# Kernel tuning notes

Measured on AMD Instinct MI355X. Metric: run time of the kernel, lower is better.

Reference implementation:

```python
import math
import jax, jax.numpy as jnp
import numpy as np

V, D, A, H, FF, L, MD = 500, 512, 512, 8, 2048, 6, 512
HD = A // H
B, S, T = 32, 512, 128


def setup_inputs() -> dict:
    key = jax.random.key(0)
    ks = jax.random.split(key, 40)
    init = lambda k, shape: (jax.random.normal(k, shape, jnp.float32) * 0.02)
    inp = {
        'memory': jax.random.normal(ks[0], (B, S, MD), jnp.float32),
        'memory_lens': jax.random.randint(ks[1], (B,), S // 2, S + 1),
        'ys_in_pad': jax.random.randint(ks[2], (B, T), 0, V),
        'ys_in_lens': jax.random.randint(ks[3], (B,), T // 2, T + 1),
        'emb': init(ks[4], (V, D)),
        'w_out': init(ks[5], (D, V)),
        'b_out': jnp.zeros((V,), jnp.float32),
        # per-layer params stacked on leading L axis (consumed by lax.scan)
        'ln_sa_g': jnp.ones((L, D), jnp.float32), 'ln_sa_b': jnp.zeros((L, D), jnp.float32),
        'sa_wq': init(ks[6], (L, D, A)), 'sa_bq': init(ks[7], (L, A)),
        'sa_wk': init(ks[8], (L, D, A)), 'sa_bk': init(ks[9], (L, A)),
        'sa_wv': init(ks[10], (L, D, A)), 'sa_bv': init(ks[11], (L, A)),
        'sa_wo': init(ks[12], (L, A, D)), 'sa_bo': init(ks[13], (L, D)),
        'ln_ca_g': jnp.ones((L, D), jnp.float32), 'ln_ca_b': jnp.zeros((L, D), jnp.float32),
        'ca_wq': init(ks[14], (L, D, A)), 'ca_bq': init(ks[15], (L, A)),
        'ca_wk': init(ks[16], (L, MD, A)), 'ca_bk': init(ks[17], (L, A)),
        'ca_wv': init(ks[18], (L, MD, A)), 'ca_bv': init(ks[19], (L, A)),
        'ca_wo': init(ks[20], (L, A, D)), 'ca_bo': init(ks[21], (L, D)),
        'ln_ff_g': jnp.ones((L, D), jnp.float32), 'ln_ff_b': jnp.zeros((L, D), jnp.float32),
        'ff_w1': init(ks[22], (L, D, FF)), 'ff_b1': init(ks[23], (L, FF)),
        'ff_w2': init(ks[24], (L, FF, D)), 'ff_b2': init(ks[25], (L, D)),
    }
    return inp


def _layernorm(x, g, b, eps=1e-5):
    m = jnp.mean(x, axis=-1, keepdims=True)
    v = jnp.mean(jnp.square(x - m), axis=-1, keepdims=True)
    return (x - m) * jax.lax.rsqrt(v + eps) * g + b


def _mha(q_in, k_in, v_in, mask, wq, bq, wk, bk, wv, bv, wo, bo):
    # mask: True = disallowed. (B, T, S) for self-attn, (B, 1, S) for cross-attn.
    b_, tq, _ = q_in.shape
    ts = k_in.shape[1]
    q = (q_in @ wq + bq).reshape(b_, tq, H, HD).transpose(0, 2, 1, 3)
    k = (k_in @ wk + bk).reshape(b_, ts, H, HD).transpose(0, 2, 1, 3)
    v = (v_in @ wv + bv).reshape(b_, ts, H, HD).transpose(0, 2, 1, 3)
    s = jnp.einsum('bhtd,bhsd->bhts', q, k) / math.sqrt(HD)
    # penalize_abs_values_gt(limit=50, penalty=1e-4) is identity in the forward
    # pass (it only injects an auxiliary gradient during training).
    s = jnp.where(mask[:, None, :, :], -jnp.inf, s)
    a = jax.nn.softmax(s, axis=-1)  # dropout p=0.0 in this config
    o = jnp.einsum('bhts,bhsd->bhtd', a, v).transpose(0, 2, 1, 3).reshape(b_, tq, A)
    return o @ wo + bo


def _forward(memory, memory_lens, ys_in_pad, ys_in_lens, emb, w_out, b_out, layer_params):
    t = ys_in_pad.shape[1]
    # make_pad_mask | ~subsequent_mask  -> (B, T, T), True = masked
    pad = jnp.arange(t)[None, :] >= ys_in_lens[:, None]            # (B, T)
    causal = ~jnp.tril(jnp.ones((t, t), bool))                     # (T, T)
    tgt_mask = pad[:, None, :] | causal[None]                      # (B, T, T)
    mem_mask = (jnp.arange(memory.shape[1])[None, :] >= memory_lens[:, None])[:, None, :]

    # embedding + sinusoidal positional encoding (dropout in eval = identity)
    pos = jnp.arange(t, dtype=jnp.float32)[:, None]
    div = jnp.exp(jnp.arange(0, D, 2, dtype=jnp.float32) * (-math.log(10000.0) / D))
    pe = jnp.zeros((t, D), jnp.float32)
    pe = pe.at[:, 0::2].set(jnp.sin(pos * div)).at[:, 1::2].set(jnp.cos(pos * div))
    x = emb[ys_in_pad] * math.sqrt(D) + pe[None]

    def step(tgt, p):
        tn = _layernorm(tgt, p['ln_sa_g'], p['ln_sa_b'])
        tgt = tgt + _mha(tn, tn, tn, tgt_mask,
                         p['sa_wq'], p['sa_bq'], p['sa_wk'], p['sa_bk'],
                         p['sa_wv'], p['sa_bv'], p['sa_wo'], p['sa_bo'])
        tn = _layernorm(tgt, p['ln_ca_g'], p['ln_ca_b'])
        tgt = tgt + _mha(tn, memory, memory, mem_mask,
                         p['ca_wq'], p['ca_bq'], p['ca_wk'], p['ca_bk'],
                         p['ca_wv'], p['ca_bv'], p['ca_wo'], p['ca_bo'])
        tn = _layernorm(tgt, p['ln_ff_g'], p['ln_ff_b'])
        h = tn @ p['ff_w1'] + p['ff_b1']
        h = h * jax.nn.sigmoid(h)  # Swish
        tgt = tgt + h @ p['ff_w2'] + p['ff_b2']
        return tgt, None

    x, _ = jax.lax.scan(step, x, layer_params)
    return x @ w_out + b_out  # (B, T, V) logits


_LAYER_KEYS = ['ln_sa_g', 'ln_sa_b', 'sa_wq', 'sa_bq', 'sa_wk', 'sa_bk', 'sa_wv', 'sa_bv',
               'sa_wo', 'sa_bo', 'ln_ca_g', 'ln_ca_b', 'ca_wq', 'ca_bq', 'ca_wk', 'ca_bk',
               'ca_wv', 'ca_bv', 'ca_wo', 'ca_bo', 'ln_ff_g', 'ln_ff_b',
               'ff_w1', 'ff_b1', 'ff_w2', 'ff_b2']


def reference(memory, memory_lens, ys_in_pad, ys_in_lens, emb, w_out, b_out,
              ln_sa_g, ln_sa_b, sa_wq, sa_bq, sa_wk, sa_bk, sa_wv, sa_bv, sa_wo, sa_bo,
              ln_ca_g, ln_ca_b, ca_wq, ca_bq, ca_wk, ca_bk, ca_wv, ca_bv, ca_wo, ca_bo,
              ln_ff_g, ln_ff_b, ff_w1, ff_b1, ff_w2, ff_b2):
    loc = locals()
    layer_params = {k: loc[k] for k in _LAYER_KEYS}
    return _forward(memory, memory_lens, ys_in_pad, ys_in_lens, emb, w_out, b_out, layer_params)
```

## Files before the change

kernel.cpp:

```cpp
#include <hip/hip_runtime.h>
#include <hip/hip_bf16.h>
#include <hip/hip_fp16.h>

constexpr int Bc = 32, Sc = 512, Tc = 128, Dc = 512, Ac = 512, Hc = 8;
constexpr int HDc = 64, FFc = 2048, Lc = 6, Vc = 500;
constexpr int NTOK = Bc * Tc;
constexpr int NMEM = Bc * Sc;

typedef unsigned short u16;
typedef __attribute__((ext_vector_type(8))) short short8;
typedef __attribute__((ext_vector_type(4))) float f32x4;

__device__ __forceinline__ u16 bfc(float x) {
  __hip_bfloat16 h = __float2bfloat16(x);
  return *reinterpret_cast<u16*>(&h);
}

__device__ __forceinline__ void gload16(const void* g, void* l) {
  __builtin_amdgcn_global_load_lds(
      (const __attribute__((address_space(1))) unsigned int*)g,
      (__attribute__((address_space(3))) unsigned int*)l, 16, 0, 0);
}

template <int N>
__device__ __forceinline__ void waitv() {
  if constexpr (N == 8)      asm volatile("s_waitcnt vmcnt(8)" ::: "memory");
  else if constexpr (N == 6) asm volatile("s_waitcnt vmcnt(6)" ::: "memory");
  else if constexpr (N == 4) asm volatile("s_waitcnt vmcnt(4)" ::: "memory");
  else if constexpr (N == 3) asm volatile("s_waitcnt vmcnt(3)" ::: "memory");
  else                       asm volatile("s_waitcnt vmcnt(0)" ::: "memory");
  __builtin_amdgcn_sched_barrier(0);
}
__device__ __forceinline__ void barrier_fenced() {
  __builtin_amdgcn_s_barrier();
  __builtin_amdgcn_sched_barrier(0);
}
__device__ __forceinline__ void lgk0_barrier() {
  asm volatile("s_waitcnt lgkmcnt(0)" ::: "memory");
  __builtin_amdgcn_sched_barrier(0);
  __builtin_amdgcn_s_barrier();
  __builtin_amdgcn_sched_barrier(0);
}

__device__ __forceinline__ float wave_sum(float v) {
#pragma unroll
  for (int o = 32; o > 0; o >>= 1) v += __shfl_down(v, o);
  return v;
}
__device__ __forceinline__ float wave_max(float v) {
#pragma unroll
  for (int o = 32; o > 0; o >>= 1) v = fmaxf(v, __shfl_down(v, o));
  return v;
}

__global__ __launch_bounds__(256) void embed_pe_k(const int* __restrict__ ys,
                                                  const float* __restrict__ emb,
                                                  float* __restrict__ x) {
  int tok = blockIdx.x;
  int t = tok & (Tc - 1);
  int id = ys[tok];
  int j = threadIdx.x;
  int d0 = 2 * j;
  const float cdiv = -9.210340371976184f / (float)Dc;
  float div = expf((float)d0 * cdiv);
  float ang = (float)t * div;
  float pe0 = sinf(ang), pe1 = cosf(ang);
  const float sc = 22.627416997969522f;
  long base = (long)tok * Dc + d0;
  long ebase = (long)id * Dc + d0;
  x[base]     = emb[ebase]     * sc + pe0;
  x[base + 1] = emb[ebase + 1] * sc + pe1;
}

__global__ __launch_bounds__(256) void layernorm_k(const float* __restrict__ x,
                                                   const float* __restrict__ g,
                                                   const float* __restrict__ bta,
                                                   u16* __restrict__ out) {
  int row = blockIdx.x;
  int tid = threadIdx.x;
  const float* xr = x + (long)row * Dc;
  float2 xv = *(const float2*)(xr + tid * 2);
  float s  = xv.x + xv.y;
  float s2 = xv.x * xv.x + xv.y * xv.y;
  __shared__ float red[4], red2[4];
#pragma unroll
  for (int o = 32; o > 0; o >>= 1) {
    s  += __shfl_down(s, o);
    s2 += __shfl_down(s2, o);
  }
  if ((tid & 63) == 0) { red[tid >> 6] = s; red2[tid >> 6] = s2; }
  __syncthreads();
  float mean = (red[0] + red[1] + red[2] + red[3]) * (1.0f / Dc);
  float ms   = (red2[0] + red2[1] + red2[2] + red2[3]) * (1.0f / Dc);
  float var  = ms - mean * mean;
  float rstd = rsqrtf(var + 1e-5f);
  float dx0 = xv.x - mean, dx1 = xv.y - mean;
  ushort2 o;
  o.x = bfc(dx0 * rstd * g[2 * tid] + bta[2 * tid]);
  o.y = bfc(dx1 * rstd * g[2 * tid + 1] + bta[2 * tid + 1]);
  *(ushort2*)(out + (long)row * Dc + tid * 2) = o;
}

__global__ __launch_bounds__(256) void wtrans_k(const float* __restrict__ src,
                                                u16* __restrict__ dst,
                                                int K, int N, long srcStride, long dstStride) {
  int z = blockIdx.z;
  src += z * srcStride;
  dst += z * dstStride;
  __shared__ float t[32][33];
  int n0 = blockIdx.x * 32, k0 = blockIdx.y * 32;
  int tx = threadIdx.x & 31, ty = threadIdx.x >> 5;
#pragma unroll
  for (int i = 0; i < 4; i++) {
    int n = n0 + tx;
    t[ty + 8 * i][tx] = (n < N) ? src[(long)(k0 + ty + 8 * i) * N + n] : 0.0f;
  }
  __syncthreads();
#pragma unroll
  for (int i = 0; i < 4; i++) {
    dst[(long)(n0 + ty + 8 * i) * K + k0 + tx] = bfc(t[tx][ty + 8 * i]);
  }
}

struct PtrPack8 { const float* p[8]; };
__global__ __launch_bounds__(256) void wtrans8_k(PtrPack8 P, u16* __restrict__ Wt,
                                                 long PLW) {
  int z = blockIdx.z;
  int widx = z / 6, l = z - widx * 6;
  const float* src = P.p[widx] + (long)l * 262144;
  u16* dst = Wt + (long)widx * 262144 + (long)l * PLW;
  __shared__ float t[32][33];
  int n0 = blockIdx.x * 32, k0 = blockIdx.y * 32;
  int tx = threadIdx.x & 31, ty = threadIdx.x >> 5;
#pragma unroll
  for (int i = 0; i < 4; i++)
    t[ty + 8 * i][tx] = src[(long)(k0 + ty + 8 * i) * 512 + n0 + tx];
  __syncthreads();
#pragma unroll
  for (int i = 0; i < 4; i++)
    dst[(long)(n0 + ty + 8 * i) * 512 + k0 + tx] = bfc(t[tx][ty + 8 * i]);
}

__global__ __launch_bounds__(256) void f2b_k(const float* __restrict__ in,
                                             u16* __restrict__ out, long n) {
  long i = ((long)blockIdx.x * 256 + threadIdx.x) * 4;
  if (i >= n) return;
  float4 v = *(const float4*)(in + i);
  ushort4 o;
  o.x = bfc(v.x); o.y = bfc(v.y); o.z = bfc(v.z); o.w = bfc(v.w);
  *(ushort4*)(out + i) = o;
}

template <int BMW, int OMODE, bool BIAS, bool RES, bool SWISH, bool NCH, bool MLEN>
__global__ __launch_bounds__(256) void mgemm_k(
    const u16* __restrict__ A, const u16* __restrict__ Bt,
    const float* __restrict__ bias0, const float* __restrict__ bias1,
    const float* __restrict__ bias2,
    void* __restrict__ Cv, const float* __restrict__ R, const int* __restrict__ mlens,
    int N, int K, int lda, int ldb, int ldc, int nbi,
    long batAo, long batAi, long batBo, long batBi, long batCo, long batCi) {
  constexpr int BM = BMW * 32;
  constexpr int LPS = (BM == 128 ? 2 : 1) + 2;

  int gx = gridDim.x, gy = gridDim.y;
  int nwg = gx * gy * gridDim.z;
  int orig = blockIdx.x + gx * (blockIdx.y + gy * blockIdx.z);
  int q = nwg >> 3, r = nwg & 7, xcd = orig & 7, off = orig >> 3;
  int wgid = (xcd < r ? xcd * (q + 1) : r * (q + 1) + (xcd - r) * q) + off;
  int bxi = wgid % gx; int tmp = wgid / gx;
  int byi = tmp % gy;  int bzi = tmp / gy;

  int z = bzi;
  int bo = z / nbi, bi = z - bo * nbi;
  int m0 = byi * BM, n0 = bxi * 128;

  if constexpr (MLEN) {
    if ((m0 & 511) >= mlens[m0 >> 9]) return;
  }

  const u16* Ab = A + bo * batAo + bi * batAi;
  const u16* Bb = Bt + bo * batBo + bi * batBi;
  long coff = bo * batCo + bi * batCi;
  const float* bias = nullptr;
  if constexpr (BIAS) bias = (bi == 0) ? bias0 : ((bi == 1) ? bias1 : bias2);

  __shared__ __align__(16) u16 As[3][BM * 32];
  __shared__ __align__(16) u16 Bs[3][128 * 32];

  int tid = threadIdx.x;
  int lane = tid & 63, wid = tid >> 6;
  int wm = wid >> 1, wn = wid & 1;
  int fr = lane & 15, grp = lane >> 4;

  f32x4 acc[BMW][4];
#pragma unroll
  for (int i = 0; i < BMW; i++)
#pragma unroll
    for (int j = 0; j < 4; j++) acc[i][j] = (f32x4){0.f, 0.f, 0.f, 0.f};

  const u16* ga = Ab + (long)(m0 + (tid >> 2)) * lda + ((tid & 3) << 3);
  const u16* gb = Bb + (long)(n0 + (tid >> 2)) * ldb + ((tid & 3) << 3);

  auto STAGE = [&](int buf, int kt) {
    u16* lA = &As[buf][tid * 8];
    u16* lB = &Bs[buf][tid * 8];
    gload16(ga + kt, lA);
    if constexpr (BM == 128) gload16(ga + kt + (long)64 * lda, lA + 2048);
    gload16(gb + kt, lB);
    gload16(gb + kt + (long)64 * ldb, lB + 2048);
  };

  auto COMPUTE = [&](int buf) {
    short8 av[BMW], bv[4];
#pragma unroll
    for (int i = 0; i < BMW; i++)
      av[i] = *(const short8*)&As[buf][(wm * BMW * 16 + i * 16 + fr) * 32 + grp * 8];
#pragma unroll
    for (int j = 0; j < 4; j++)
      bv[j] = *(const short8*)&Bs[buf][(wn * 64 + j * 16 + fr) * 32 + grp * 8];
#pragma unroll
    for (int i = 0; i < BMW; i++)
#pragma unroll
      for (int j = 0; j < 4; j++)
        acc[i][j] = __builtin_amdgcn_mfma_f32_16x16x32_bf16(av[i], bv[j], acc[i][j], 0, 0, 0);
  };

  int NT = K >> 5;
  STAGE(0, 0);
  STAGE(1, 32);
  int cbuf = 0, sbuf = 2, kt = 64;
  for (int t = 0; t < NT - 2; ++t) {
    STAGE(sbuf, kt); kt += 32;
    waitv<2 * LPS>();
    barrier_fenced();
    COMPUTE(cbuf);
    lgk0_barrier();
    sbuf = cbuf; cbuf = (cbuf == 2) ? 0 : cbuf + 1;
  }
  waitv<LPS>();  barrier_fenced(); COMPUTE(cbuf); lgk0_barrier();
  cbuf = (cbuf == 2) ? 0 : cbuf + 1;
  waitv<0>();    barrier_fenced(); COMPUTE(cbuf);

  int rbase = m0 + wm * BMW * 16 + grp * 4;
  int cbase = n0 + wn * 64 + fr;
#pragma unroll
  for (int i = 0; i < BMW; i++) {
#pragma unroll
    for (int j = 0; j < 4; j++) {
      int col = cbase + j * 16;
      if (NCH && col >= N) continue;
      float bb = 0.0f;
      if constexpr (BIAS) bb = bias[col];
#pragma unroll
      for (int r2 = 0; r2 < 4; r2++) {
        int row = rbase + i * 16 + r2;
        float v = acc[i][j][r2] + bb;
        long idx = coff + (long)row * ldc + col;
        if constexpr (RES) v += R[idx];
        if constexpr (SWISH) v = v / (1.0f + expf(-v));
        if constexpr (OMODE == 0) ((u16*)Cv)[idx] = bfc(v);
        else ((float*)Cv)[idx] = v;
      }
    }
  }
}

template <int SKV, int KVBLK, bool CAUSAL, int IQ>
__global__ __launch_bounds__(256) void fattn_k(
    const u16* __restrict__ Q, const u16* __restrict__ Kg, const u16* __restrict__ Vg,
    u16* __restrict__ O, const int* __restrict__ lens) {
  constexpr int NJ  = KVBLK / 16;
  constexpr int NKV = KVBLK / 32;
  constexpr int NT  = SKV / KVBLK;
  constexpr int KST = 72;
  constexpr int VST = KVBLK + 8;
  constexpr int WR  = 16 * IQ;
  constexpr int WGR = 64 * IQ;
  constexpr int CH  = KVBLK / 32;

  __shared__ __align__(16) u16 Ks[KVBLK * KST];
  __shared__ __align__(16) u16 Vs[64 * VST];
  __shared__ __align__(16) u16 Ps[WGR * VST];

  int bh = blockIdx.x; int b = bh >> 3, h = bh & 7;
  int row00 = blockIdx.y * WGR;
  int tid = threadIdx.x, lane = tid & 63, wid = tid >> 6;
  int fr = lane & 15, grp = lane >> 4;
  int len = lens[b];
  int row0w = row00 + wid * WR;

  short8 qa[IQ][2];
  {
    const u16* qp = Q + ((long)b * Tc + row0w + fr) * 512 + h * 64 + grp * 8;
#pragma unroll
    for (int i = 0; i < IQ; i++)
#pragma unroll
      for (int k2 = 0; k2 < 2; k2++)
        qa[i][k2] = *(const short8*)(qp + (long)i * 16 * 512 + k2 * 32);
  }

  float m_run[IQ][4], l_run[IQ][4];
  f32x4 acc_o[IQ][4];
#pragma unroll
  for (int i = 0; i < IQ; i++)
#pragma unroll
    for (int r = 0; r < 4; r++) { m_run[i][r] = -1e30f; l_run[i][r] = 0.0f; }
#pragma unroll
  for (int i = 0; i < IQ; i++)
#pragma unroll
    for (int j = 0; j < 4; j++) acc_o[i][j] = (f32x4){0.f, 0.f, 0.f, 0.f};

  const u16* Kbase = Kg + ((long)b * SKV) * 512 + h * 64;
  const u16* Vbase = Vg + ((long)b * SKV) * 512 + h * 64;

  int NTeff = NT;
  if constexpr (CAUSAL) NTeff = (row00 + WGR - 1) / KVBLK + 1;
  int lenT = (len + KVBLK - 1) / KVBLK;
  if (lenT < NTeff) NTeff = lenT;

  short8 kreg[CH], vreg[CH];
#pragma unroll
  for (int c = 0; c < CH; c++) {
    int idx = tid + 256 * c; int kv = idx >> 3, s = idx & 7;
    kreg[c] = *(const short8*)(Kbase + (long)kv * 512 + s * 8);
    vreg[c] = *(const short8*)(Vbase + (long)kv * 512 + s * 8);
  }

  for (int t = 0; t < NTeff; t++) {
    int kv0 = t * KVBLK;
    __syncthreads();
#pragma unroll
    for (int c = 0; c < CH; c++) {
      int idx = tid + 256 * c; int kv = idx >> 3, s = idx & 7;
      *(short8*)&Ks[kv * KST + s * 8] = kreg[c];
#pragma unroll
      for (int j = 0; j < 8; j++)
        Vs[(s * 8 + j) * VST + kv] = (u16)vreg[c][j];
    }
    __syncthreads();
    if (t + 1 < NTeff) {
      int kvn = kv0 + KVBLK;
#pragma unroll
      for (int c = 0; c < CH; c++) {
        int idx = tid + 256 * c; int kv = idx >> 3, s = idx & 7;
        kreg[c] = *(const short8*)(Kbase + (long)(kvn + kv) * 512 + s * 8);
        vreg[c] = *(const short8*)(Vbase + (long)(kvn + kv) * 512 + s * 8);
      }
    }

    int jmax = NJ;
    if constexpr (CAUSAL) {
      jmax = (row0w + WR - 1 - kv0) / 16 + 1;
      if (jmax > NJ) jmax = NJ;
    }

    f32x4 accs[IQ][NJ];
    __builtin_amdgcn_s_setprio(1);
#pragma unroll
    for (int j = 0; j < NJ; j++) {
      if (CAUSAL && j >= jmax) continue;
      short8 bv0 = *(const short8*)&Ks[(j * 16 + fr) * KST + grp * 8];
      short8 bv1 = *(const short8*)&Ks[(j * 16 + fr) * KST + 32 + grp * 8];
#pragma unroll
      for (int i = 0; i < IQ; i++) {
        f32x4 a = __builtin_amdgcn_mfma_f32_16x16x32_bf16(qa[i][0], bv0, (f32x4){0.f,0.f,0.f,0.f}, 0, 0, 0);
        accs[i][j] = __builtin_amdgcn_mfma_f32_16x16x32_bf16(qa[i][1], bv1, a, 0, 0, 0);
      }
    }
    __builtin_amdgcn_s_setprio(0);

    float alpha[IQ][4];
#pragma unroll
    for (int i = 0; i < IQ; i++) {
#pragma unroll
      for (int r = 0; r < 4; r++) {
        int qrow = row0w + i * 16 + grp * 4 + r;
        float vmax = -1e30f;
#pragma unroll
        for (int j = 0; j < NJ; j++) {
          if (CAUSAL && j >= jmax) continue;
          int kvb = kv0 + j * 16 + fr;
          float s = accs[i][j][r] * 0.125f;
          bool msk = (kvb >= len) || (CAUSAL && kvb > qrow);
          s = msk ? -1e30f : s;
          accs[i][j][r] = s;
          vmax = fmaxf(vmax, s);
        }
        vmax = fmaxf(vmax, __shfl_xor(vmax, 1));
        vmax = fmaxf(vmax, __shfl_xor(vmax, 2));
        vmax = fmaxf(vmax, __shfl_xor(vmax, 4));
        vmax = fmaxf(vmax, __shfl_xor(vmax, 8));
        float mn = fmaxf(m_run[i][r], vmax);
        float al = __expf(m_run[i][r] - mn);
        m_run[i][r] = mn;
        alpha[i][r] = al;
        float rs = 0.0f;
#pragma unroll
        for (int j = 0; j < NJ; j++) {
          if (CAUSAL && j >= jmax) continue;
          float p = __expf(accs[i][j][r] - mn);
          accs[i][j][r] = p;
          rs += p;
        }
        rs += __shfl_xor(rs, 1);
        rs += __shfl_xor(rs, 2);
        rs += __shfl_xor(rs, 4);
        rs += __shfl_xor(rs, 8);
        l_run[i][r] = l_run[i][r] * al + rs;
      }
    }

#pragma unroll
    for (int i = 0; i < IQ; i++)
#pragma unroll
      for (int j = 0; j < NJ; j++) {
        if (CAUSAL && j >= jmax) continue;
#pragma unroll
        for (int r = 0; r < 4; r++) {
          int prow = wid * WR + i * 16 + grp * 4 + r;
          Ps[prow * VST + j * 16 + fr] = bfc(accs[i][j][r]);
        }
      }

#pragma unroll
    for (int i = 0; i < IQ; i++)
#pragma unroll
      for (int jd = 0; jd < 4; jd++)
#pragma unroll
        for (int r = 0; r < 4; r++)
          acc_o[i][jd][r] *= alpha[i][r];

    int kvmax = NKV;
    if constexpr (CAUSAL) {
      kvmax = (row0w + WR - 1 - kv0) / 32 + 1;
      if (kvmax > NKV) kvmax = NKV;
    }
    __builtin_amdgcn_s_setprio(1);
#pragma unroll
    for (int kk = 0; kk < NKV; kk++) {
      if (CAUSAL && kk >= kvmax) continue;
      short8 pa[IQ];
#pragma unroll
      for (int i = 0; i < IQ; i++)
        pa[i] = *(const short8*)&Ps[(wid * WR + i * 16 + fr) * VST + kk * 32 + grp * 8];
#pragma unroll
      for (int jd = 0; jd < 4; jd++) {
        short8 vb = *(const short8*)&Vs[(jd * 16 + fr) * VST + kk * 32 + grp * 8];
#pragma unroll
        for (int i = 0; i < IQ; i++)
          acc_o[i][jd] = __builtin_amdgcn_mfma_f32_16x16x32_bf16(pa[i], vb, acc_o[i][jd], 0, 0, 0);
      }
    }
    __builtin_amdgcn_s_setprio(0);
  }

#pragma unroll
  for (int i = 0; i < IQ; i++) {
#pragma unroll
    for (int r = 0; r < 4; r++) {
      float inv = 1.0f / l_run[i][r];
      long tok = (long)b * Tc + row0w + i * 16 + grp * 4 + r;
#pragma unroll
      for (int jd = 0; jd < 4; jd++)
        O[tok * 512 + h * 64 + jd * 16 + fr] = bfc(acc_o[i][jd][r] * inv);
    }
  }
}

extern "C" void kernel_launch(void* const* d_in, const int* in_sizes, int n_in,
                              void* d_out, int out_size, void* d_ws, size_t ws_size,
                              hipStream_t stream) {
  const float* memory   = (const float*)d_in[0];
  const int*   mem_lens = (const int*)d_in[1];
  const int*   ys       = (const int*)d_in[2];
  const int*   ys_lens  = (const int*)d_in[3];
  const float* emb      = (const float*)d_in[4];
  const float* w_out    = (const float*)d_in[5];
  const float* b_out    = (const float*)d_in[6];
  const float* pp[26];
  for (int i = 0; i < 26; i++) pp[i] = (const float*)d_in[7 + i];

  constexpr long PLW = 4194304;
  constexpr long OFF_SAQ = 0, OFF_SAK = 262144, OFF_SAV = 524288, OFF_SAO = 786432,
                 OFF_CAQ = 1048576, OFF_CAK = 1310720, OFF_CAV = 1572864,
                 OFF_CAO = 1835008, OFF_FF1 = 2097152, OFF_FF2 = 3145728,
                 OFF_WOUT = 6 * PLW;
  u16*   Wt   = (u16*)d_ws;
  float* X    = (float*)(Wt + 25427968);
  u16*   TO   = (u16*)(X + 2097152);
  u16*   QKV  = TO + 2097152;
  u16*   memb = QKV + 3 * 2097152;
  u16*   Kb   = memb + 8388608;
  u16*   SCR  = Kb + 8388608;
  float* OUT  = (float*)d_out;

  PtrPack8 P8;
  P8.p[0] = pp[2];  P8.p[1] = pp[4];  P8.p[2] = pp[6];  P8.p[3] = pp[8];
  P8.p[4] = pp[12]; P8.p[5] = pp[14]; P8.p[6] = pp[16]; P8.p[7] = pp[18];
  wtrans8_k<<<dim3(16, 16, 48), 256, 0, stream>>>(P8, Wt, PLW);
  wtrans_k<<<dim3(64, 16, Lc), 256, 0, stream>>>(pp[22], Wt + OFF_FF1, 512, 2048, 1048576, PLW);
  wtrans_k<<<dim3(16, 64, Lc), 256, 0, stream>>>(pp[24], Wt + OFF_FF2, 2048, 512, 1048576, PLW);
  wtrans_k<<<dim3(16, 16, 1), 256, 0, stream>>>(w_out, Wt + OFF_WOUT, 512, 500, 0, 0);

  f2b_k<<<(NMEM * Dc / 4 + 255) / 256, 256, 0, stream>>>(memory, memb, (long)NMEM * Dc);
  embed_pe_k<<<NTOK, 256, 0, stream>>>(ys, emb, X);

  for (int l = 0; l < Lc; l++) {
    const u16* WtL = Wt + (long)l * PLW;

    layernorm_k<<<NTOK, 256, 0, stream>>>(X, pp[0] + (long)l * Dc, pp[1] + (long)l * Dc, TO);
    mgemm_k<4, 0, true, false, false, false, false><<<dim3(4, 32, 3), 256, 0, stream>>>(
        TO, WtL + OFF_SAQ, pp[3] + (long)l * Ac, pp[5] + (long)l * Ac, pp[7] + (long)l * Ac,
        QKV, nullptr, nullptr, 512, 512, 512, 512, 512, 3, 0, 0, 0, 262144, 0, 2097152);
    fattn_k<128, 128, true, 2><<<dim3(256, 1), 256, 0, stream>>>(
        QKV, QKV + 2097152, QKV + 2 * 2097152, TO, ys_lens);
    mgemm_k<2, 1, true, true, false, false, false><<<dim3(4, 64, 1), 256, 0, stream>>>(
        TO, WtL + OFF_SAO, pp[9] + (long)l * Dc, nullptr, nullptr, X, X, nullptr,
        512, 512, 512, 512, 512, 1, 0, 0, 0, 0, 0, 0);

    layernorm_k<<<NTOK, 256, 0, stream>>>(X, pp[10] + (long)l * Dc, pp[11] + (long)l * Dc, TO);
    mgemm_k<2, 0, true, false, false, false, false><<<dim3(4, 64, 1), 256, 0, stream>>>(
        TO, WtL + OFF_CAQ, pp[13] + (long)l * Ac, nullptr, nullptr, QKV, nullptr, nullptr,
        512, 512, 512, 512, 512, 1, 0, 0, 0, 0, 0, 0);
    mgemm_k<4, 0, true, false, false, false, true><<<dim3(4, 128, 2), 256, 0, stream>>>(
        memb, WtL + OFF_CAK, pp[15] + (long)l * Ac, pp[17] + (long)l * Ac, nullptr,
        Kb, nullptr, mem_lens, 512, 512, 512, 512, 512, 2, 0, 0, 0, 262144, 0, 8388608);
    fattn_k<512, 128, false, 1><<<dim3(256, 2), 256, 0, stream>>>(
        QKV, Kb, SCR, TO, mem_lens);
    mgemm_k<2, 1, true, true, false, false, false><<<dim3(4, 64, 1), 256, 0, stream>>>(
        TO, WtL + OFF_CAO, pp[19] + (long)l * Dc, nullptr, nullptr, X, X, nullptr,
        512, 512, 512, 512, 512, 1, 0, 0, 0, 0, 0, 0);

    layernorm_k<<<NTOK, 256, 0, stream>>>(X, pp[20] + (long)l * Dc, pp[21] + (long)l * Dc, TO);
    mgemm_k<4, 0, true, false, true, false, false><<<dim3(16, 32, 1), 256, 0, stream>>>(
        TO, WtL + OFF_FF1, pp[23] + (long)l * FFc, nullptr, nullptr, SCR, nullptr, nullptr,
        2048, 512, 512, 512, 2048, 1, 0, 0, 0, 0, 0, 0);
    mgemm_k<2, 1, true, true, false, false, false><<<dim3(4, 64, 1), 256, 0, stream>>>(
        SCR, WtL + OFF_FF2, pp[25] + (long)l * Dc, nullptr, nullptr, X, X, nullptr,
        512, 2048, 2048, 2048, 512, 1, 0, 0, 0, 0, 0, 0);
  }

  f2b_k<<<(NTOK * Dc / 4 + 255) / 256, 256, 0, stream>>>(X, TO, (long)NTOK * Dc);
  mgemm_k<2, 1, true, false, false, true, false><<<dim3(4, 64, 1), 256, 0, stream>>>(
      TO, Wt + OFF_WOUT, b_out, nullptr, nullptr, OUT, nullptr, nullptr,
      500, 512, 512, 512, 500, 1, 0, 0, 0, 0, 0, 0);
}
```

Baseline: 1.185 ms.

## Deepen GEMM pipeline to 4 stages, merge cross-attn Q/KV GEMMs, split causal attention

The GEMM kernel moves from triple to quadruple LDS buffering, keeping three tiles in flight to hide more global-load latency. The cross-attention Q projection and the memory K/V projections are merged into one launch with a MERGE mode that selects input and output per z-slice. Causal self-attention now runs with one query tile per wave over a two-dimensional grid, zeroing masked P columns so the PV loop stays aligned. In exchange, LDS use grows, which may lower occupancy, and the merged launch contains idle blocks for Q rows beyond 4096.

```diff
diff --git a/kernel.cpp b/kernel.cpp
--- a/kernel.cpp
+++ b/kernel.cpp
@@ -24,7 +24,9 @@
 
 template <int N>
 __device__ __forceinline__ void waitv() {
-  if constexpr (N == 8)      asm volatile("s_waitcnt vmcnt(8)" ::: "memory");
+  if constexpr (N == 12)     asm volatile("s_waitcnt vmcnt(12)" ::: "memory");
+  else if constexpr (N == 9) asm volatile("s_waitcnt vmcnt(9)" ::: "memory");
+  else if constexpr (N == 8) asm volatile("s_waitcnt vmcnt(8)" ::: "memory");
   else if constexpr (N == 6) asm volatile("s_waitcnt vmcnt(6)" ::: "memory");
   else if constexpr (N == 4) asm volatile("s_waitcnt vmcnt(4)" ::: "memory");
   else if constexpr (N == 3) asm volatile("s_waitcnt vmcnt(3)" ::: "memory");
@@ -45,11 +47,6 @@
 __device__ __forceinline__ float wave_sum(float v) {
 #pragma unroll
   for (int o = 32; o > 0; o >>= 1) v += __shfl_down(v, o);
-  return v;
-}
-__device__ __forceinline__ float wave_max(float v) {
-#pragma unroll
-  for (int o = 32; o > 0; o >>= 1) v = fmaxf(v, __shfl_down(v, o));
   return v;
 }
 
@@ -151,12 +148,13 @@
   *(ushort4*)(out + i) = o;
 }
 
-template <int BMW, int OMODE, bool BIAS, bool RES, bool SWISH, bool NCH, bool MLEN>
+template <int BMW, int OMODE, bool BIAS, bool RES, bool SWISH, bool NCH, bool MLEN, bool MERGE>
 __global__ __launch_bounds__(256) void mgemm_k(
     const u16* __restrict__ A, const u16* __restrict__ Bt,
     const float* __restrict__ bias0, const float* __restrict__ bias1,
     const float* __restrict__ bias2,
     void* __restrict__ Cv, const float* __restrict__ R, const int* __restrict__ mlens,
+    const u16* __restrict__ A2, void* __restrict__ Cv2, int Mq,
     int N, int K, int lda, int ldb, int ldc, int nbi,
     long batAo, long batAi, long batBo, long batBi, long batCo, long batCi) {
   constexpr int BM = BMW * 32;
@@ -174,18 +172,33 @@
   int bo = z / nbi, bi = z - bo * nbi;
   int m0 = byi * BM, n0 = bxi * 128;
 
-  if constexpr (MLEN) {
-    if ((m0 & 511) >= mlens[m0 >> 9]) return;
-  }
-
-  const u16* Ab = A + bo * batAo + bi * batAi;
+  const u16* Ab;
+  long coff;
+  void* Cbase;
+  if constexpr (MERGE) {
+    if (bi == 0) {
+      if (m0 >= Mq) return;
+      Ab = A + (long)0;
+      coff = 0; Cbase = Cv;
+    } else {
+      if (MLEN && (m0 & 511) >= mlens[m0 >> 9]) return;
+      Ab = A2;
+      coff = (long)(bi - 1) * batCi; Cbase = Cv2;
+    }
+  } else {
+    if constexpr (MLEN) {
+      if ((m0 & 511) >= mlens[m0 >> 9]) return;
+    }
+    Ab = A + bo * batAo + bi * batAi;
+    coff = bo * batCo + bi * batCi;
+    Cbase = Cv;
+  }
   const u16* Bb = Bt + bo * batBo + bi * batBi;
-  long coff = bo * batCo + bi * batCi;
   const float* bias = nullptr;
   if constexpr (BIAS) bias = (bi == 0) ? bias0 : ((bi == 1) ? bias1 : bias2);
 
-  __shared__ __align__(16) u16 As[3][BM * 32];
-  __shared__ __align__(16) u16 Bs[3][128 * 32];
+  __shared__ __align__(16) u16 As[4][BM * 32];
+  __shared__ __align__(16) u16 Bs[4][128 * 32];
 
   int tid = threadIdx.x;
   int lane = tid & 63, wid = tid >> 6;
@@ -228,18 +241,18 @@
   int NT = K >> 5;
   STAGE(0, 0);
   STAGE(1, 32);
-  int cbuf = 0, sbuf = 2, kt = 64;
-  for (int t = 0; t < NT - 2; ++t) {
-    STAGE(sbuf, kt); kt += 32;
-    waitv<2 * LPS>();
+  STAGE(2, 64);
+  int kt = 96;
+  for (int t = 0; t < NT - 3; ++t) {
+    STAGE((t + 3) & 3, kt); kt += 32;
+    waitv<3 * LPS>();
     barrier_fenced();
-    COMPUTE(cbuf);
+    COMPUTE(t & 3);
     lgk0_barrier();
-    sbuf = cbuf; cbuf = (cbuf == 2) ? 0 : cbuf + 1;
-  }
-  waitv<LPS>();  barrier_fenced(); COMPUTE(cbuf); lgk0_barrier();
-  cbuf = (cbuf == 2) ? 0 : cbuf + 1;
-  waitv<0>();    barrier_fenced(); COMPUTE(cbuf);
+  }
+  waitv<2 * LPS>(); barrier_fenced(); COMPUTE((NT - 3) & 3); lgk0_barrier();
+  waitv<LPS>();     barrier_fenced(); COMPUTE((NT - 2) & 3); lgk0_barrier();
+  waitv<0>();       barrier_fenced(); COMPUTE((NT - 1) & 3);
 
   int rbase = m0 + wm * BMW * 16 + grp * 4;
   int cbase = n0 + wn * 64 + fr;
@@ -258,8 +271,8 @@
         long idx = coff + (long)row * ldc + col;
         if constexpr (RES) v += R[idx];
         if constexpr (SWISH) v = v / (1.0f + expf(-v));
-        if constexpr (OMODE == 0) ((u16*)Cv)[idx] = bfc(v);
-        else ((float*)Cv)[idx] = v;
+        if constexpr (OMODE == 0) ((u16*)Cbase)[idx] = bfc(v);
+        else ((float*)Cbase)[idx] = v;
       }
     }
   }
@@ -315,6 +328,7 @@
 
   int NTeff = NT;
   if constexpr (CAUSAL) NTeff = (row00 + WGR - 1) / KVBLK + 1;
+  if (NTeff > NT) NTeff = NT;
   int lenT = (len + KVBLK - 1) / KVBLK;
   if (lenT < NTeff) NTeff = lenT;
 
@@ -348,10 +362,14 @@
       }
     }
 
-    int jmax = NJ;
+    int jmax = NJ, kvmax = NKV, jmaxW = NJ;
     if constexpr (CAUSAL) {
       jmax = (row0w + WR - 1 - kv0) / 16 + 1;
       if (jmax > NJ) jmax = NJ;
+      kvmax = (row0w + WR - 1 - kv0) / 32 + 1;
+      if (kvmax > NKV) kvmax = NKV;
+      jmaxW = 2 * kvmax;
+      if (jmaxW > NJ) jmaxW = NJ;
     }
 
     f32x4 accs[IQ][NJ];
@@ -414,11 +432,12 @@
     for (int i = 0; i < IQ; i++)
 #pragma unroll
       for (int j = 0; j < NJ; j++) {
-        if (CAUSAL && j >= jmax) continue;
+        if (CAUSAL && j >= jmaxW) continue;
 #pragma unroll
         for (int r = 0; r < 4; r++) {
           int prow = wid * WR + i * 16 + grp * 4 + r;
-          Ps[prow * VST + j * 16 + fr] = bfc(accs[i][j][r]);
+          float pv = (CAUSAL && j >= jmax) ? 0.0f : accs[i][j][r];
+          Ps[prow * VST + j * 16 + fr] = bfc(pv);
         }
       }
 
@@ -430,11 +449,6 @@
         for (int r = 0; r < 4; r++)
           acc_o[i][jd][r] *= alpha[i][r];
 
-    int kvmax = NKV;
-    if constexpr (CAUSAL) {
-      kvmax = (row0w + WR - 1 - kv0) / 32 + 1;
-      if (kvmax > NKV) kvmax = NKV;
-    }
     __builtin_amdgcn_s_setprio(1);
 #pragma unroll
     for (int kk = 0; kk < NKV; kk++) {
@@ -509,39 +523,43 @@
     const u16* WtL = Wt + (long)l * PLW;
 
     layernorm_k<<<NTOK, 256, 0, stream>>>(X, pp[0] + (long)l * Dc, pp[1] + (long)l * Dc, TO);
-    mgemm_k<4, 0, true, false, false, false, false><<<dim3(4, 32, 3), 256, 0, stream>>>(
+    mgemm_k<4, 0, true, false, false, false, false, false><<<dim3(4, 32, 3), 256, 0, stream>>>(
         TO, WtL + OFF_SAQ, pp[3] + (long)l * Ac, pp[5] + (long)l * Ac, pp[7] + (long)l * Ac,
-        QKV, nullptr, nullptr, 512, 512, 512, 512, 512, 3, 0, 0, 0, 262144, 0, 2097152);
-    fattn_k<128, 128, true, 2><<<dim3(256, 1), 256, 0, stream>>>(
+        QKV, nullptr, nullptr, nullptr, nullptr, 0,
+        512, 512, 512, 512, 512, 3, 0, 0, 0, 262144, 0, 2097152);
+    fattn_k<128, 128, true, 1><<<dim3(256, 2), 256, 0, stream>>>(
         QKV, QKV + 2097152, QKV + 2 * 2097152, TO, ys_lens);
-    mgemm_k<2, 1, true, true, false, false, false><<<dim3(4, 64, 1), 256, 0, stream>>>(
+    mgemm_k<2, 1, true, true, false, false, false, false><<<dim3(4, 64, 1), 256, 0, stream>>>(
         TO, WtL + OFF_SAO, pp[9] + (long)l * Dc, nullptr, nullptr, X, X, nullptr,
+        nullptr, nullptr, 0,
         512, 512, 512, 512, 512, 1, 0, 0, 0, 0, 0, 0);
 
     layernorm_k<<<NTOK, 256, 0, stream>>>(X, pp[10] + (long)l * Dc, pp[11] + (long)l * Dc, TO);
-    mgemm_k<2, 0, true, false, false, false, false><<<dim3(4, 64, 1), 256, 0, stream>>>(
-        TO, WtL + OFF_CAQ, pp[13] + (long)l * Ac, nullptr, nullptr, QKV, nullptr, nullptr,
-        512, 512, 512, 512, 512, 1, 0, 0, 0, 0, 0, 0);
-    mgemm_k<4, 0, true, false, false, false, true><<<dim3(4, 128, 2), 256, 0, stream>>>(
-        memb, WtL + OFF_CAK, pp[15] + (long)l * Ac, pp[17] + (long)l * Ac, nullptr,
-        Kb, nullptr, mem_lens, 512, 512, 512, 512, 512, 2, 0, 0, 0, 262144, 0, 8388608);
+    mgemm_k<4, 0, true, false, false, false, true, true><<<dim3(4, 128, 3), 256, 0, stream>>>(
+        TO, WtL + OFF_CAQ, pp[13] + (long)l * Ac, pp[15] + (long)l * Ac, pp[17] + (long)l * Ac,
+        QKV, nullptr, mem_lens, memb, Kb, 4096,
+        512, 512, 512, 512, 512, 3, 0, 0, 0, 262144, 0, 8388608);
     fattn_k<512, 128, false, 1><<<dim3(256, 2), 256, 0, stream>>>(
         QKV, Kb, SCR, TO, mem_lens);
-    mgemm_k<2, 1, true, true, false, false, false><<<dim3(4, 64, 1), 256, 0, stream>>>(
+    mgemm_k<2, 1, true, true, false, false, false, false><<<dim3(4, 64, 1), 256, 0, stream>>>(
         TO, WtL + OFF_CAO, pp[19] + (long)l * Dc, nullptr, nullptr, X, X, nullptr,
+        nullptr, nullptr, 0,
         512, 512, 512, 512, 512, 1, 0, 0, 0, 0, 0, 0);
 
     layernorm_k<<<NTOK, 256, 0, stream>>>(X, pp[20] + (long)l * Dc, pp[21] + (long)l * Dc, TO);
-    mgemm_k<4, 0, true, false, true, false, false><<<dim3(16, 32, 1), 256, 0, stream>>>(
+    mgemm_k<4, 0, true, false, true, false, false, false><<<dim3(16, 32, 1), 256, 0, stream>>>(
         TO, WtL + OFF_FF1, pp[23] + (long)l * FFc, nullptr, nullptr, SCR, nullptr, nullptr,
+        nullptr, nullptr, 0,
         2048, 512, 512, 512, 2048, 1, 0, 0, 0, 0, 0, 0);
-    mgemm_k<2, 1, true, true, false, false, false><<<dim3(4, 64, 1), 256, 0, stream>>>(
+    mgemm_k<2, 1, true, true, false, false, false, false><<<dim3(4, 64, 1), 256, 0, stream>>>(
         SCR, WtL + OFF_FF2, pp[25] + (long)l * Dc, nullptr, nullptr, X, X, nullptr,
+        nullptr, nullptr, 0,
         512, 2048, 2048, 2048, 512, 1, 0, 0, 0, 0, 0, 0);
   }
 
   f2b_k<<<(NTOK * Dc / 4 + 255) / 256, 256, 0, stream>>>(X, TO, (long)NTOK * Dc);
-  mgemm_k<2, 1, true, false, false, true, false><<<dim3(4, 64, 1), 256, 0, stream>>>(
+  mgemm_k<2, 1, true, false, false, true, false, false><<<dim3(4, 64, 1), 256, 0, stream>>>(
       TO, Wt + OFF_WOUT, b_out, nullptr, nullptr, OUT, nullptr, nullptr,
+      nullptr, nullptr, 0,
       500, 512, 512, 512, 500, 1, 0, 0, 0, 0, 0, 0);
 }
```

Measured after the change: 1.234 ms. 4.1% more time.
